# Kernel optimization log

Measured on AMD Instinct MI355X. Metric: run time of the kernel, lower is better.

The kernel has to match this reference:

```python
import jax, jax.numpy as jnp
import numpy as np
import math

D_MODEL = 1024
N_HEADS = 16
D_HEAD = D_MODEL // N_HEADS
DECAY_MAX = 0.99  # buggy torch init: only the LAST head's decay rate survives the loop
LN_EPS = 1e-5


def setup_inputs() -> dict:
    key = jax.random.key(0)
    ks = jax.random.split(key, 12)
    B, S = 2, 2048
    x = jax.random.normal(ks[0], (B, S, D_MODEL), dtype=jnp.float32)
    def w(k):
        return jax.random.normal(k, (D_MODEL, D_MODEL), dtype=jnp.float32) * 0.02
    return {
        "x": x,
        "Wq": w(ks[1]), "bq": jnp.zeros((D_MODEL,), jnp.float32),
        "Wk": w(ks[2]), "bk": jnp.zeros((D_MODEL,), jnp.float32),
        "Wv": w(ks[3]), "bv": jnp.zeros((D_MODEL,), jnp.float32),
        "Wg": w(ks[4]), "bg": jnp.zeros((D_MODEL,), jnp.float32),
        "Wo": w(ks[5]), "bo": jnp.zeros((D_MODEL,), jnp.float32),
        "gamma": jnp.ones((D_MODEL,), jnp.float32),
        "beta": jnp.zeros((D_MODEL,), jnp.float32),
    }


def _decay_mask(S):
    # faithful to torch buffer: decay_matrix[i,j] = DECAY_MAX**(i-j) for j<=i else 0
    i = jnp.arange(S, dtype=jnp.float32)[:, None]
    j = jnp.arange(S, dtype=jnp.float32)[None, :]
    diff = i - j
    return jnp.where(diff >= 0, jnp.power(jnp.float32(DECAY_MAX), diff), 0.0)  # [S,S]


def reference(x, Wq, bq, Wk, bk, Wv, bv, Wg, bg, Wo, bo, gamma, beta):
    B, S, D = x.shape
    H, DH = N_HEADS, D_HEAD
    # projections -> [B,H,S,DH]
    Q = (x @ Wq + bq).reshape(B, S, H, DH).transpose(0, 2, 1, 3)
    K = (x @ Wk + bk).reshape(B, S, H, DH).transpose(0, 2, 1, 3)
    V = (x @ Wv + bv).reshape(B, S, H, DH).transpose(0, 2, 1, 3)
    scores = jnp.einsum('bhsd,bhtd->bhst', Q, K) / math.sqrt(DH)  # [B,H,S,S]
    mask = _decay_mask(S)  # [S,S], broadcast over B,H (head-independent per torch bug)
    retained = jnp.einsum('bhst,bhtd->bhsd', scores * mask, V)
    retained = retained.transpose(0, 2, 1, 3).reshape(B, S, D)
    # LayerNorm over last dim
    mu = jnp.mean(retained, axis=-1, keepdims=True)
    var = jnp.var(retained, axis=-1, keepdims=True)
    normed = (retained - mu) * jax.lax.rsqrt(var + LN_EPS) * gamma + beta
    G = jax.nn.sigmoid(x @ Wg + bg)
    return (normed * G) @ Wo + bo  # dropout = identity (eval)
```

## Files before the change

kernel.cpp:

```cpp
#include <hip/hip_runtime.h>

typedef __attribute__((ext_vector_type(4))) float f32x4;
typedef __attribute__((ext_vector_type(8))) short bf16x8;
typedef unsigned short USHORT;

static __device__ __forceinline__ float bf2f(USHORT u) {
    return __uint_as_float(((unsigned)u) << 16);
}
static __device__ __forceinline__ USHORT f2bf(float f) {
    unsigned u = __float_as_uint(f);
    unsigned r = u + 0x7FFF + ((u >> 16) & 1);
    return (USHORT)(r >> 16);
}

#define GLDS16(gp, lp) __builtin_amdgcn_global_load_lds(                      \
    (const __attribute__((address_space(1))) unsigned int*)(gp),              \
    (__attribute__((address_space(3))) unsigned int*)(lp), 16, 0, 0)

#define FULL_BARRIER() asm volatile("s_waitcnt vmcnt(0) lgkmcnt(0)\ns_barrier" ::: "memory")

#define D64 0.52559648f
#define L2D (-0.014499569695115089f)

struct PrepArgs { const float* src[5]; USHORT* dst[5]; const float* x; USHORT* xb; };

__global__ __launch_bounds__(256) void k_prep(PrepArgs pa) {
    const int z = blockIdx.z;
    const int tid = threadIdx.x;
    __shared__ USHORT t[64][65];
    if (z < 5) {
        const float* __restrict__ W  = pa.src[z];
        USHORT* __restrict__      WT = pa.dst[z];
        const int k0 = blockIdx.y * 64, n0 = blockIdx.x * 64;
#pragma unroll
        for (int s = 0; s < 4; s++) {
            int slot = tid + s * 256;
            int row = slot >> 4, c4 = (slot & 15) * 4;
            float4 vv = *(const float4*)&W[(size_t)(k0 + row) * 1024 + n0 + c4];
            t[row][c4 + 0] = f2bf(vv.x);
            t[row][c4 + 1] = f2bf(vv.y);
            t[row][c4 + 2] = f2bf(vv.z);
            t[row][c4 + 3] = f2bf(vv.w);
        }
        __syncthreads();
#pragma unroll
        for (int s = 0; s < 2; s++) {
            int slot = tid + s * 256;
            int n = slot >> 3, c8 = (slot & 7) * 8;
            USHORT tmp[8];
#pragma unroll
            for (int u = 0; u < 8; u++) tmp[u] = t[c8 + u][n];
            *(int4*)&WT[(size_t)(n0 + n) * 1024 + k0 + c8] = *(int4*)tmp;
        }
    } else {
        const int bi = blockIdx.y * 16 + blockIdx.x;
        const float* xs = pa.x + (size_t)bi * 16384;
        USHORT* xd = pa.xb + (size_t)bi * 16384;
#pragma unroll
        for (int u = 0; u < 16; u++) {
            int idx = u * 1024 + tid * 4;
            float4 v = *(const float4*)&xs[idx];
            *(ushort4*)&xd[idx] = make_ushort4(f2bf(v.x), f2bf(v.y), f2bf(v.z), f2bf(v.w));
        }
    }
}

struct GArgs {
    const USHORT* A;
    const USHORT* W[4];
    const float*  bias[4];
    void*         dst[4];
    USHORT*       dstv;
    float         scale[4];
    int           mode[4];
};

__global__ __launch_bounds__(256, 2) void k_gemm(GArgs ga) {
    const int z = blockIdx.z;
    const USHORT* __restrict__ A  = ga.A;
    const USHORT* __restrict__ BT = ga.W[z];
    __shared__ USHORT As[2][128 * 32];
    __shared__ USHORT Bs[2][128 * 32];
    const int tid = threadIdx.x;
    const int m0 = blockIdx.y * 128, n0 = blockIdx.x * 128;
    const int w = tid >> 6, l = tid & 63, lr = l & 15, q = l >> 4;
    const int wr = w >> 1, wc = w & 1;
    const int srow = tid >> 2, sco = (tid & 3) * 8;
    f32x4 acc[4][4] = {};
    GLDS16(&A [(size_t)(m0 + srow)      * 1024 + sco], &As[0][srow * 32 + sco]);
    GLDS16(&A [(size_t)(m0 + srow + 64) * 1024 + sco], &As[0][(srow + 64) * 32 + sco]);
    GLDS16(&BT[(size_t)(n0 + srow)      * 1024 + sco], &Bs[0][srow * 32 + sco]);
    GLDS16(&BT[(size_t)(n0 + srow + 64) * 1024 + sco], &Bs[0][(srow + 64) * 32 + sco]);
    for (int kt = 0; kt < 32; kt++) {
        const int cur = kt & 1;
        FULL_BARRIER();
        if (kt + 1 < 32) {
            const int k1 = (kt + 1) * 32;
            const int nxt = 1 - cur;
            GLDS16(&A [(size_t)(m0 + srow)      * 1024 + k1 + sco], &As[nxt][srow * 32 + sco]);
            GLDS16(&A [(size_t)(m0 + srow + 64) * 1024 + k1 + sco], &As[nxt][(srow + 64) * 32 + sco]);
            GLDS16(&BT[(size_t)(n0 + srow)      * 1024 + k1 + sco], &Bs[nxt][srow * 32 + sco]);
            GLDS16(&BT[(size_t)(n0 + srow + 64) * 1024 + k1 + sco], &Bs[nxt][(srow + 64) * 32 + sco]);
        }
        bf16x8 af[4], bfr[4];
#pragma unroll
        for (int mi = 0; mi < 4; mi++)
            af[mi] = *(const bf16x8*)&As[cur][(wr * 64 + mi * 16 + lr) * 32 + q * 8];
#pragma unroll
        for (int ni = 0; ni < 4; ni++)
            bfr[ni] = *(const bf16x8*)&Bs[cur][(wc * 64 + ni * 16 + lr) * 32 + q * 8];
#pragma unroll
        for (int mi = 0; mi < 4; mi++)
#pragma unroll
            for (int ni = 0; ni < 4; ni++)
                acc[mi][ni] = __builtin_amdgcn_mfma_f32_16x16x32_bf16(
                    af[mi], bfr[ni], acc[mi][ni], 0, 0, 0);
    }
    const float scale = ga.scale[z];
    const int mode = ga.mode[z];
    const float* __restrict__ bias = ga.bias[z];
#pragma unroll
    for (int ni = 0; ni < 4; ni++) {
        int col = n0 + wc * 64 + ni * 16 + lr;
        float bv = bias[col];
#pragma unroll
        for (int mi = 0; mi < 4; mi++) {
            int r0 = m0 + wr * 64 + mi * 16 + q * 4;
            float vr[4];
#pragma unroll
            for (int r = 0; r < 4; r++) {
                float v = acc[mi][ni][r] + bv;
                if (mode == 1) v = 1.0f / (1.0f + __expf(-v));
                vr[r] = v * scale;
            }
            if (mode == 3) {
                float* df = (float*)ga.dst[z];
#pragma unroll
                for (int r = 0; r < 4; r++)
                    df[(size_t)(r0 + r) * 1024 + col] = vr[r];
            } else if (mode == 2) {
                int b = r0 >> 11, s = r0 & 2047;
                int h = col >> 6, d = col & 63;
                const float NP1 = 1.0101010101010102f;
                float c0 = exp2f(-L2D * (float)(s & 63));
                float c1 = c0 * NP1, c2 = c1 * NP1, c3 = c2 * NP1;
                *(ushort4*)&ga.dstv[(size_t)(((b * 16 + h) * 64) + d) * 2048 + s] =
                    make_ushort4(f2bf(vr[0] * c0), f2bf(vr[1] * c1),
                                 f2bf(vr[2] * c2), f2bf(vr[3] * c3));
            } else {
                USHORT* db = (USHORT*)ga.dst[z];
#pragma unroll
                for (int r = 0; r < 4; r++)
                    db[(size_t)(r0 + r) * 1024 + col] = f2bf(vr[r]);
            }
        }
    }
}

#define LDSA(buf, kh) (((buf) * 2 + (kh)) * 8192)
#define LDSB(buf, kh) (32768 + ((buf) * 2 + (kh)) * 8192)
#define BAR() asm volatile("s_barrier" ::: "memory")
#define VM8() asm volatile("s_waitcnt vmcnt(8)" ::: "memory")

#define STAGE_A(ks, kh, buf) do {                                             \
    const USHORT* s_ = aBase + (ks) * 64 + (kh) * 32;                         \
    GLDS16(s_,          &lds[LDSA(buf, kh) + ldsT]);                          \
    GLDS16(s_ + 131072, &lds[LDSA(buf, kh) + 4096 + ldsT]); } while (0)

#define STAGE_B(ks, kh, buf) do {                                             \
    const USHORT* s_ = bBase + (ks) * 64 + (kh) * 32;                         \
    GLDS16(s_,          &lds[LDSB(buf, kh) + ldsT]);                          \
    GLDS16(s_ + 131072, &lds[LDSB(buf, kh) + 4096 + ldsT]); } while (0)

#define PHASE256(buf, kh, mg, LOADB, STAGE_STMT, WAITSTMT) do {               \
    _Pragma("unroll")                                                         \
    for (int mi = 0; mi < 4; mi++)                                            \
        af[mi] = *(const bf16x8*)&lds[LDSA(buf, kh) + aoff + ((mg) * 4 + mi) * 512]; \
    if (LOADB) {                                                              \
        _Pragma("unroll")                                                     \
        for (int ni = 0; ni < 4; ni++)                                        \
            bfrag[ni] = *(const bf16x8*)&lds[LDSB(buf, kh) + boff + ni * 512];\
    }                                                                         \
    STAGE_STMT;                                                               \
    BAR();                                                                    \
    __builtin_amdgcn_s_setprio(1);                                            \
    _Pragma("unroll")                                                         \
    for (int mi = 0; mi < 4; mi++)                                            \
        _Pragma("unroll")                                                     \
        for (int ni = 0; ni < 4; ni++)                                        \
            acc[(mg) * 4 + mi][ni] = __builtin_amdgcn_mfma_f32_16x16x32_bf16( \
                af[mi], bfrag[ni], acc[(mg) * 4 + mi][ni], 0, 0, 0);          \
    __builtin_amdgcn_s_setprio(0);                                            \
    WAITSTMT;                                                                 \
    BAR();                                                                    \
} while (0)

__global__ __launch_bounds__(512, 2) void k_gemm256(GArgs ga) {
    extern __shared__ USHORT lds[];
    int bid = blockIdx.x + 4 * (blockIdx.y + 16 * blockIdx.z);
    bid = (bid & 7) * 32 + (bid >> 3);
    const int bz = bid >> 6;
    const int by = (bid >> 2) & 15;
    const int bx = bid & 3;
    const int z = bz;
    const USHORT* __restrict__ A  = ga.A;
    const USHORT* __restrict__ BT = ga.W[z];
    const int m0 = by * 256, n0 = bx * 256;
    const int tid = threadIdx.x;
    const int wid = tid >> 6, l = tid & 63, lr = l & 15, q = l >> 4;
    const int wr = wid >> 2, wc = wid & 3;
    const int srow = tid >> 2;
    const int scol = (((tid & 3) ^ ((tid >> 2) & 3)) << 3);
    const USHORT* aBase = A  + (size_t)(m0 + srow) * 1024 + scol;
    const USHORT* bBase = BT + (size_t)(n0 + srow) * 1024 + scol;
    const int ldsT = tid * 8;
    const int kread = ((q ^ (lr & 3)) << 3);
    const int aoff = (wr * 128 + lr) * 32 + kread;
    const int boff = (wc * 64 + lr) * 32 + kread;
    f32x4 acc[8][4] = {};
    bf16x8 af[4], bfrag[4];

    STAGE_A(0, 0, 0); STAGE_B(0, 0, 0);
    STAGE_A(0, 1, 0); STAGE_B(0, 1, 0);
    STAGE_A(1, 0, 1); STAGE_B(1, 0, 1);
    VM8();
    BAR();

    for (int kt = 0; kt < 16; kt += 2) {
        const int ks1 = kt + 1;
        const int ks2 = (kt + 2 < 16) ? kt + 2 : 15;
        const int ks3 = (kt + 2 < 16) ? kt + 2 : 15;
        const int ks4 = (kt + 3 < 16) ? kt + 3 : 15;
        PHASE256(0, 0, 0, 1, STAGE_A(ks1, 1, 1), (void)0);
        PHASE256(0, 0, 1, 0, STAGE_B(ks1, 1, 1), VM8());
        PHASE256(0, 1, 0, 1, STAGE_A(ks2, 0, 0), (void)0);
        PHASE256(0, 1, 1, 0, STAGE_B(ks2, 0, 0), VM8());
        PHASE256(1, 0, 0, 1, STAGE_A(ks3, 1, 0), (void)0);
        PHASE256(1, 0, 1, 0, STAGE_B(ks3, 1, 0), VM8());
        PHASE256(1, 1, 0, 1, STAGE_A(ks4, 0, 1), (void)0);
        PHASE256(1, 1, 1, 0, STAGE_B(ks4, 0, 1), VM8());
    }

    const float scale = ga.scale[z];
    const int mode = ga.mode[z];
    const float* __restrict__ bias = ga.bias[z];
#pragma unroll
    for (int ni = 0; ni < 4; ni++) {
        int col = n0 + wc * 64 + ni * 16 + lr;
        float bv = bias[col];
#pragma unroll
        for (int mi = 0; mi < 8; mi++) {
            int r0 = m0 + wr * 128 + mi * 16 + q * 4;
            float vr[4];
#pragma unroll
            for (int r = 0; r < 4; r++) {
                float v = acc[mi][ni][r] + bv;
                if (mode == 1) v = 1.0f / (1.0f + __expf(-v));
                vr[r] = v * scale;
            }
            if (mode == 3) {
                float* df = (float*)ga.dst[z];
#pragma unroll
                for (int r = 0; r < 4; r++)
                    df[(size_t)(r0 + r) * 1024 + col] = vr[r];
            } else if (mode == 2) {
                int b = r0 >> 11, s = r0 & 2047;
                int h = col >> 6, d = col & 63;
                const float NP1 = 1.0101010101010102f;
                float c0 = exp2f(-L2D * (float)(s & 63));
                float c1 = c0 * NP1, c2 = c1 * NP1, c3 = c2 * NP1;
                *(ushort4*)&ga.dstv[(size_t)(((b * 16 + h) * 64) + d) * 2048 + s] =
                    make_ushort4(f2bf(vr[0] * c0), f2bf(vr[1] * c1),
                                 f2bf(vr[2] * c2), f2bf(vr[3] * c3));
            } else {
                USHORT* db = (USHORT*)ga.dst[z];
#pragma unroll
                for (int r = 0; r < 4; r++)
                    db[(size_t)(r0 + r) * 1024 + col] = f2bf(vr[r]);
            }
        }
    }
}

__global__ __launch_bounds__(256) void k_attn_u(const USHORT* __restrict__ K,
                                                const USHORT* __restrict__ VT,
                                                float* __restrict__ U) {
    const int bh = blockIdx.x, c = blockIdx.y;
    const int b = bh >> 4, h = bh & 15;
    const int tid = threadIdx.x, w = tid >> 6, l = tid & 63, lr = l & 15, q = l >> 4;
    __shared__ USHORT KT[64 * 72];
    __shared__ USHORT Vs[64 * 72];
#pragma unroll
    for (int s = 0; s < 2; s++) {
        int slot = tid + s * 256;
        int row = slot >> 3, co = (slot & 7) * 8;
        USHORT kv[8];
        *(int4*)kv = *(const int4*)&K[(size_t)(b * 2048 + c * 64 + row) * 1024 + h * 64 + co];
#pragma unroll
        for (int u = 0; u < 8; u++) KT[(co + u) * 72 + row] = kv[u];
        *(int4*)&Vs[row * 72 + co] =
            *(const int4*)&VT[(size_t)(bh * 64 + row) * 2048 + c * 64 + co];
    }
    __syncthreads();
    f32x4 acc[4] = {};
    bf16x8 av[2];
#pragma unroll
    for (int kk = 0; kk < 2; kk++)
        av[kk] = *(const bf16x8*)&Vs[(w * 16 + lr) * 72 + kk * 32 + q * 8];
#pragma unroll
    for (int dkt = 0; dkt < 4; dkt++)
#pragma unroll
        for (int kk = 0; kk < 2; kk++) {
            bf16x8 bk = *(const bf16x8*)&KT[(dkt * 16 + lr) * 72 + kk * 32 + q * 8];
            acc[dkt] = __builtin_amdgcn_mfma_f32_16x16x32_bf16(av[kk], bk, acc[dkt], 0, 0, 0);
        }
    float* slot = U + (size_t)(bh * 32 + c) * 4096;
#pragma unroll
    for (int dkt = 0; dkt < 4; dkt++)
#pragma unroll
        for (int r = 0; r < 4; r++)
            slot[(w * 16 + q * 4 + r) * 64 + dkt * 16 + lr] = acc[dkt][r] * D64;
}

__global__ __launch_bounds__(256, 2) void k_apply(const USHORT* __restrict__ Q,
                                                  const USHORT* __restrict__ K,
                                                  const USHORT* __restrict__ VT,
                                                  const float* __restrict__ U,
                                                  USHORT* __restrict__ R,
                                                  float* __restrict__ stats) {
    const int bh = blockIdx.x, c = blockIdx.y;
    const int b = bh >> 4, h = bh & 15;
    const int i0 = c * 64;
    const int tid = threadIdx.x, w = tid >> 6, l = tid & 63, lr = l & 15, q = l >> 4;
    __shared__ USHORT Qs[64 * 72];
    __shared__ USHORT Ks[64 * 72];
    __shared__ USHORT Vs[64 * 72];
    __shared__ USHORT Ps[4][16 * 72];
    __shared__ unsigned Spk[4096];
#pragma unroll
    for (int s = 0; s < 2; s++) {
        int slot = tid + s * 256;
        int row = slot >> 3, c8 = (slot & 7) * 8;
        USHORT q8[8];
        *(int4*)q8 = *(const int4*)&Q[(size_t)(b * 2048 + i0 + row) * 1024 + h * 64 + c8];
        const float fr = exp2f(L2D * (float)row);
#pragma unroll
        for (int u = 0; u < 8; u++) q8[u] = f2bf(bf2f(q8[u]) * fr);
        *(int4*)&Qs[row * 72 + c8] = *(int4*)q8;
        *(int4*)&Ks[row * 72 + c8] =
            *(const int4*)&K[(size_t)(b * 2048 + i0 + row) * 1024 + h * 64 + c8];
        *(int4*)&Vs[row * 72 + c8] =
            *(const int4*)&VT[(size_t)(bh * 64 + row) * 2048 + i0 + c8];
    }
    if (c > 0) {
        float sa[16] = {};
        const float* Ub = U + (size_t)bh * 32 * 4096 + tid * 16;
        for (int cp = 0; cp < c; cp++) {
            const float* p = Ub + (size_t)cp * 4096;
#pragma unroll
            for (int u4 = 0; u4 < 4; u4++) {
                float4 uv = *(const float4*)(p + u4 * 4);
                sa[u4 * 4 + 0] = sa[u4 * 4 + 0] * D64 + uv.x;
                sa[u4 * 4 + 1] = sa[u4 * 4 + 1] * D64 + uv.y;
                sa[u4 * 4 + 2] = sa[u4 * 4 + 2] * D64 + uv.z;
                sa[u4 * 4 + 3] = sa[u4 * 4 + 3] * D64 + uv.w;
            }
        }
#pragma unroll
        for (int u = 0; u < 16; u++) {
            USHORT hi = f2bf(sa[u]);
            float  lo = sa[u] - bf2f(hi);
            Spk[tid * 16 + u] = (unsigned)hi | ((unsigned)f2bf(lo) << 16);
        }
    }
    __syncthreads();
    bf16x8 bqf[2];
#pragma unroll
    for (int kk = 0; kk < 2; kk++)
        bqf[kk] = *(const bf16x8*)&Qs[(w * 16 + lr) * 72 + kk * 32 + q * 8];
    f32x4 accr[4] = {};
    if (c > 0) {
#pragma unroll
        for (int dt = 0; dt < 4; dt++)
#pragma unroll
            for (int kk = 0; kk < 2; kk++) {
                const unsigned* sp = &Spk[(dt * 16 + lr) * 64 + kk * 32 + q * 8];
                uint4 pa = *(const uint4*)sp;
                uint4 pb = *(const uint4*)(sp + 4);
                unsigned pk[8] = { pa.x, pa.y, pa.z, pa.w, pb.x, pb.y, pb.z, pb.w };
                bf16x8 hi, lo;
#pragma unroll
                for (int u = 0; u < 8; u++) {
                    hi[u] = (short)(pk[u] & 0xffffu);
                    lo[u] = (short)(pk[u] >> 16);
                }
                accr[dt] = __builtin_amdgcn_mfma_f32_16x16x32_bf16(hi, bqf[kk], accr[dt], 0, 0, 0);
                accr[dt] = __builtin_amdgcn_mfma_f32_16x16x32_bf16(lo, bqf[kk], accr[dt], 0, 0, 0);
            }
    }
    {
        f32x4 accp[4] = {};
#pragma unroll
        for (int kk = 0; kk < 2; kk++)
#pragma unroll
            for (int jt = 0; jt < 4; jt++) {
                bf16x8 akf = *(const bf16x8*)&Ks[(jt * 16 + lr) * 72 + kk * 32 + q * 8];
                accp[jt] = __builtin_amdgcn_mfma_f32_16x16x32_bf16(akf, bqf[kk], accp[jt], 0, 0, 0);
            }
        const int ii = w * 16 + lr;
#pragma unroll
        for (int jt = 0; jt < 4; jt++) {
            const int jj = jt * 16 + q * 4;
            float v0 = (jj + 0 <= ii) ? accp[jt][0] : 0.0f;
            float v1 = (jj + 1 <= ii) ? accp[jt][1] : 0.0f;
            float v2 = (jj + 2 <= ii) ? accp[jt][2] : 0.0f;
            float v3 = (jj + 3 <= ii) ? accp[jt][3] : 0.0f;
            unsigned w0 = __builtin_amdgcn_perm(
                __float_as_uint(v1), __float_as_uint(v0), 0x07060302u);
            unsigned w1 = __builtin_amdgcn_perm(
                __float_as_uint(v3), __float_as_uint(v2), 0x07060302u);
            *(uint2*)&Ps[w][lr * 72 + jt * 16 + q * 4] = make_uint2(w0, w1);
        }
        asm volatile("s_waitcnt lgkmcnt(0)" ::: "memory");
#pragma unroll
        for (int kk = 0; kk < 2; kk++) {
            bf16x8 bpf = *(const bf16x8*)&Ps[w][lr * 72 + kk * 32 + q * 8];
#pragma unroll
            for (int dt = 0; dt < 4; dt++) {
                bf16x8 avf = *(const bf16x8*)&Vs[(dt * 16 + lr) * 72 + kk * 32 + q * 8];
                accr[dt] = __builtin_amdgcn_mfma_f32_16x16x32_bf16(avf, bpf, accr[dt], 0, 0, 0);
            }
        }
    }
    {
        float s1 = 0.f, s2 = 0.f;
#pragma unroll
        for (int dt = 0; dt < 4; dt++)
#pragma unroll
            for (int r = 0; r < 4; r++) {
                float v = accr[dt][r];
                s1 += v; s2 += v * v;
            }
        s1 += __shfl_down(s1, 32); s2 += __shfl_down(s2, 32);
        s1 += __shfl_down(s1, 16); s2 += __shfl_down(s2, 16);
        if (q == 0) {
            int row = b * 2048 + i0 + w * 16 + lr;
            *(float2*)&stats[((size_t)row * 16 + h) * 2] = make_float2(s1, s2);
        }
    }
    {
        const int i = i0 + w * 16 + lr;
#pragma unroll
        for (int dt = 0; dt < 4; dt++) {
            f32x4 a = accr[dt];
            *(ushort4*)&R[(size_t)(b * 2048 + i) * 1024 + h * 64 + dt * 16 + q * 4] =
                make_ushort4(f2bf(a[0]), f2bf(a[1]), f2bf(a[2]), f2bf(a[3]));
        }
    }
}

__global__ __launch_bounds__(256) void k_ln_gate(const USHORT* __restrict__ R,
                                                 const USHORT* __restrict__ G,
                                                 const float* __restrict__ stats,
                                                 const float* __restrict__ gamma,
                                                 const float* __restrict__ beta,
                                                 USHORT* __restrict__ NG) {
    const int row = blockIdx.x, tid = threadIdx.x;
    float s1 = 0.f, s2 = 0.f;
    const float* sp = &stats[(size_t)row * 32];
#pragma unroll
    for (int hh = 0; hh < 8; hh++) {
        float4 v = *(const float4*)(sp + hh * 4);
        s1 += v.x + v.z; s2 += v.y + v.w;
    }
    const float mu  = s1 * (1.0f / 1024.0f);
    const float var = s2 * (1.0f / 1024.0f) - mu * mu;
    const float inv = rsqrtf(fmaxf(var, 0.0f) + 1e-5f);
    ushort4 rv = *(const ushort4*)&R[(size_t)row * 1024 + tid * 4];
    ushort4 g4 = *(const ushort4*)&G[(size_t)row * 1024 + tid * 4];
    float4 gm = *(const float4*)&gamma[tid * 4];
    float4 bt = *(const float4*)&beta[tid * 4];
    float  vv[4]  = { bf2f(rv.x), bf2f(rv.y), bf2f(rv.z), bf2f(rv.w) };
    USHORT gg[4]  = { g4.x, g4.y, g4.z, g4.w };
    float  gmm[4] = { gm.x, gm.y, gm.z, gm.w };
    float  btt[4] = { bt.x, bt.y, bt.z, bt.w };
    USHORT o4[4];
#pragma unroll
    for (int u = 0; u < 4; u++) {
        float nv = (vv[u] - mu) * inv * gmm[u] + btt[u];
        o4[u] = f2bf(nv * bf2f(gg[u]));
    }
    *(ushort4*)&NG[(size_t)row * 1024 + tid * 4] = make_ushort4(o4[0], o4[1], o4[2], o4[3]);
}

extern "C" void kernel_launch(void* const* d_in, const int* in_sizes, int n_in,
                              void* d_out, int out_size, void* d_ws, size_t ws_size,
                              hipStream_t stream) {
    const float* x     = (const float*)d_in[0];
    const float* Wq    = (const float*)d_in[1];
    const float* bq    = (const float*)d_in[2];
    const float* Wk    = (const float*)d_in[3];
    const float* bk    = (const float*)d_in[4];
    const float* Wv    = (const float*)d_in[5];
    const float* bv    = (const float*)d_in[6];
    const float* Wg    = (const float*)d_in[7];
    const float* bg    = (const float*)d_in[8];
    const float* Wo    = (const float*)d_in[9];
    const float* bo    = (const float*)d_in[10];
    const float* gamma = (const float*)d_in[11];
    const float* beta  = (const float*)d_in[12];

    char* ws = (char*)d_ws;
    const size_t MB = 1 << 20;
    USHORT* WqT = (USHORT*)(ws + 0 * MB);
    USHORT* WkT = (USHORT*)(ws + 2 * MB);
    USHORT* WvT = (USHORT*)(ws + 4 * MB);
    USHORT* WgT = (USHORT*)(ws + 6 * MB);
    USHORT* WoT = (USHORT*)(ws + 8 * MB);
    USHORT* Qb  = (USHORT*)(ws + 10 * MB);
    USHORT* Kb  = (USHORT*)(ws + 18 * MB);
    USHORT* VTb = (USHORT*)(ws + 26 * MB);
    USHORT* Gb  = (USHORT*)(ws + 34 * MB);
    float*  Sts = (float*) (ws + 42 * MB);
    USHORT* NGb = Qb;
    USHORT* Xb  = (USHORT*)d_out;
    float*  Ust = (float*)d_out;

    {
        PrepArgs pa;
        pa.src[0] = Wq; pa.src[1] = Wk; pa.src[2] = Wv; pa.src[3] = Wg; pa.src[4] = Wo;
        pa.dst[0] = WqT; pa.dst[1] = WkT; pa.dst[2] = WvT; pa.dst[3] = WgT; pa.dst[4] = WoT;
        pa.x = x; pa.xb = Xb;
        k_prep<<<dim3(16, 16, 6), 256, 0, stream>>>(pa);
    }
    {
        static int s_256ok = -1;
        if (s_256ok < 0) {
            hipError_t e = hipFuncSetAttribute(
                reinterpret_cast<const void*>(&k_gemm256),
                hipFuncAttributeMaxDynamicSharedMemorySize, 131072);
            s_256ok = (e == hipSuccess) ? 1 : 0;
        }
        GArgs ga;
        ga.A = Xb;
        ga.W[0] = WqT; ga.W[1] = WkT; ga.W[2] = WvT; ga.W[3] = WgT;
        ga.bias[0] = bq; ga.bias[1] = bk; ga.bias[2] = bv; ga.bias[3] = bg;
        ga.dst[0] = Qb; ga.dst[1] = Kb; ga.dst[2] = nullptr; ga.dst[3] = Gb;
        ga.dstv = VTb;
        ga.scale[0] = 0.125f; ga.scale[1] = 1.0f; ga.scale[2] = 1.0f; ga.scale[3] = 1.0f;
        ga.mode[0] = 0; ga.mode[1] = 0; ga.mode[2] = 2; ga.mode[3] = 1;
        if (s_256ok)
            k_gemm256<<<dim3(4, 16, 4), 512, 131072, stream>>>(ga);
        else
            k_gemm<<<dim3(8, 32, 4), 256, 0, stream>>>(ga);
    }
    k_attn_u<<<dim3(32, 32), 256, 0, stream>>>(Kb, VTb, Ust);
    k_apply<<<dim3(32, 32), 256, 0, stream>>>(Qb, Kb, VTb, Ust, Kb, Sts);
    k_ln_gate<<<4096, 256, 0, stream>>>(Kb, Gb, Sts, gamma, beta, NGb);
    {
        GArgs go;
        go.A = NGb;
        for (int i = 0; i < 4; i++) {
            go.W[i] = WoT; go.bias[i] = bo; go.dst[i] = d_out;
            go.scale[i] = 1.0f; go.mode[i] = 3;
        }
        go.dstv = nullptr;
        k_gemm<<<dim3(8, 32, 1), 256, 0, stream>>>(go);
    }
}
```

Before: 221.2 us.

## Add prefix-scan kernel for chunk states and fix LDS swizzle pattern

Adds a separate k_scan kernel that turns the per-chunk KV state contributions into decayed prefix sums in place. k_apply then reads a single precomputed state instead of re-accumulating all previous chunks, which removes quadratic redundant reads of U. The change also alters the XOR swizzle used for LDS staging and reads in both GEMM kernels, and adds it to the 128-tile GEMM, to reduce bank conflicts. It costs one extra kernel launch and a serial 32-step scan over U.

```diff
diff --git a/kernel.cpp b/kernel.cpp
--- a/kernel.cpp
+++ b/kernel.cpp
@@ -74,6 +74,7 @@
     float         scale[4];
     int           mode[4];
 };
+
 
 __global__ __launch_bounds__(256, 2) void k_gemm(GArgs ga) {
     const int z = blockIdx.z;
@@ -86,29 +87,31 @@
     const int w = tid >> 6, l = tid & 63, lr = l & 15, q = l >> 4;
     const int wr = w >> 1, wc = w & 1;
     const int srow = tid >> 2, sco = (tid & 3) * 8;
+    const int scol = (((tid & 3) ^ ((tid >> 3) & 3)) << 3);
+    const int kread = ((q ^ ((lr >> 1) & 3)) << 3);
     f32x4 acc[4][4] = {};
-    GLDS16(&A [(size_t)(m0 + srow)      * 1024 + sco], &As[0][srow * 32 + sco]);
-    GLDS16(&A [(size_t)(m0 + srow + 64) * 1024 + sco], &As[0][(srow + 64) * 32 + sco]);
-    GLDS16(&BT[(size_t)(n0 + srow)      * 1024 + sco], &Bs[0][srow * 32 + sco]);
-    GLDS16(&BT[(size_t)(n0 + srow + 64) * 1024 + sco], &Bs[0][(srow + 64) * 32 + sco]);
+    GLDS16(&A [(size_t)(m0 + srow)      * 1024 + scol], &As[0][srow * 32 + sco]);
+    GLDS16(&A [(size_t)(m0 + srow + 64) * 1024 + scol], &As[0][(srow + 64) * 32 + sco]);
+    GLDS16(&BT[(size_t)(n0 + srow)      * 1024 + scol], &Bs[0][srow * 32 + sco]);
+    GLDS16(&BT[(size_t)(n0 + srow + 64) * 1024 + scol], &Bs[0][(srow + 64) * 32 + sco]);
     for (int kt = 0; kt < 32; kt++) {
         const int cur = kt & 1;
         FULL_BARRIER();
         if (kt + 1 < 32) {
             const int k1 = (kt + 1) * 32;
             const int nxt = 1 - cur;
-            GLDS16(&A [(size_t)(m0 + srow)      * 1024 + k1 + sco], &As[nxt][srow * 32 + sco]);
-            GLDS16(&A [(size_t)(m0 + srow + 64) * 1024 + k1 + sco], &As[nxt][(srow + 64) * 32 + sco]);
-            GLDS16(&BT[(size_t)(n0 + srow)      * 1024 + k1 + sco], &Bs[nxt][srow * 32 + sco]);
-            GLDS16(&BT[(size_t)(n0 + srow + 64) * 1024 + k1 + sco], &Bs[nxt][(srow + 64) * 32 + sco]);
+            GLDS16(&A [(size_t)(m0 + srow)      * 1024 + k1 + scol], &As[nxt][srow * 32 + sco]);
+            GLDS16(&A [(size_t)(m0 + srow + 64) * 1024 + k1 + scol], &As[nxt][(srow + 64) * 32 + sco]);
+            GLDS16(&BT[(size_t)(n0 + srow)      * 1024 + k1 + scol], &Bs[nxt][srow * 32 + sco]);
+            GLDS16(&BT[(size_t)(n0 + srow + 64) * 1024 + k1 + scol], &Bs[nxt][(srow + 64) * 32 + sco]);
         }
         bf16x8 af[4], bfr[4];
 #pragma unroll
         for (int mi = 0; mi < 4; mi++)
-            af[mi] = *(const bf16x8*)&As[cur][(wr * 64 + mi * 16 + lr) * 32 + q * 8];
+            af[mi] = *(const bf16x8*)&As[cur][(wr * 64 + mi * 16 + lr) * 32 + kread];
 #pragma unroll
         for (int ni = 0; ni < 4; ni++)
-            bfr[ni] = *(const bf16x8*)&Bs[cur][(wc * 64 + ni * 16 + lr) * 32 + q * 8];
+            bfr[ni] = *(const bf16x8*)&Bs[cur][(wc * 64 + ni * 16 + lr) * 32 + kread];
 #pragma unroll
         for (int mi = 0; mi < 4; mi++)
 #pragma unroll
@@ -210,11 +213,11 @@
     const int wid = tid >> 6, l = tid & 63, lr = l & 15, q = l >> 4;
     const int wr = wid >> 2, wc = wid & 3;
     const int srow = tid >> 2;
-    const int scol = (((tid & 3) ^ ((tid >> 2) & 3)) << 3);
+    const int scol = (((tid & 3) ^ ((tid >> 3) & 3)) << 3);
     const USHORT* aBase = A  + (size_t)(m0 + srow) * 1024 + scol;
     const USHORT* bBase = BT + (size_t)(n0 + srow) * 1024 + scol;
     const int ldsT = tid * 8;
-    const int kread = ((q ^ (lr & 3)) << 3);
+    const int kread = ((q ^ ((lr >> 1) & 3)) << 3);
     const int aoff = (wr * 128 + lr) * 32 + kread;
     const int boff = (wc * 64 + lr) * 32 + kread;
     f32x4 acc[8][4] = {};
@@ -320,6 +323,22 @@
 #pragma unroll
         for (int r = 0; r < 4; r++)
             slot[(w * 16 + q * 4 + r) * 64 + dkt * 16 + lr] = acc[dkt][r] * D64;
+}
+
+__global__ __launch_bounds__(256) void k_scan(float* __restrict__ U) {
+    const int bh = blockIdx.x;
+    const int idx4 = blockIdx.y * 256 + threadIdx.x;
+    float* base = U + (size_t)bh * 32 * 4096 + idx4 * 4;
+    float4 s = make_float4(0.f, 0.f, 0.f, 0.f);
+    for (int c = 0; c < 32; c++) {
+        float* p = base + (size_t)c * 4096;
+        float4 v = *(const float4*)p;
+        s.x = s.x * D64 + v.x;
+        s.y = s.y * D64 + v.y;
+        s.z = s.z * D64 + v.z;
+        s.w = s.w * D64 + v.w;
+        *(float4*)p = s;
+    }
 }
 
 __global__ __launch_bounds__(256, 2) void k_apply(const USHORT* __restrict__ Q,
@@ -353,18 +372,13 @@
             *(const int4*)&VT[(size_t)(bh * 64 + row) * 2048 + i0 + c8];
     }
     if (c > 0) {
-        float sa[16] = {};
-        const float* Ub = U + (size_t)bh * 32 * 4096 + tid * 16;
-        for (int cp = 0; cp < c; cp++) {
-            const float* p = Ub + (size_t)cp * 4096;
-#pragma unroll
-            for (int u4 = 0; u4 < 4; u4++) {
-                float4 uv = *(const float4*)(p + u4 * 4);
-                sa[u4 * 4 + 0] = sa[u4 * 4 + 0] * D64 + uv.x;
-                sa[u4 * 4 + 1] = sa[u4 * 4 + 1] * D64 + uv.y;
-                sa[u4 * 4 + 2] = sa[u4 * 4 + 2] * D64 + uv.z;
-                sa[u4 * 4 + 3] = sa[u4 * 4 + 3] * D64 + uv.w;
-            }
+        const float* p = U + (size_t)(bh * 32 + (c - 1)) * 4096 + tid * 16;
+        float sa[16];
+#pragma unroll
+        for (int u4 = 0; u4 < 4; u4++) {
+            float4 uv = *(const float4*)(p + u4 * 4);
+            sa[u4 * 4 + 0] = uv.x; sa[u4 * 4 + 1] = uv.y;
+            sa[u4 * 4 + 2] = uv.z; sa[u4 * 4 + 3] = uv.w;
         }
 #pragma unroll
         for (int u = 0; u < 16; u++) {
@@ -555,6 +569,7 @@
             k_gemm<<<dim3(8, 32, 4), 256, 0, stream>>>(ga);
     }
     k_attn_u<<<dim3(32, 32), 256, 0, stream>>>(Kb, VTb, Ust);
+    k_scan<<<dim3(32, 4), 256, 0, stream>>>(Ust);
     k_apply<<<dim3(32, 32), 256, 0, stream>>>(Qb, Kb, VTb, Ust, Kb, Sts);
     k_ln_gate<<<4096, 256, 0, stream>>>(Kb, Gb, Sts, gamma, beta, NGb);
     {
```

Measured after the change: 214.4 us. 1.03x faster.
